# Performance work log

Measured on AMD Instinct MI355X. Metric: run time of the kernel, lower is better.

The kernel has to match this reference:

```python
import jax, jax.numpy as jnp
import numpy as np

EMBED = 1024
HEADS = 16
HEAD_DIM = EMBED // HEADS


def setup_inputs() -> dict:
    key = jax.random.key(0)
    ks = jax.random.split(key, 7)
    N, S = 2, 2048
    k = jax.random.normal(ks[0], (N, S, EMBED), dtype=jnp.float32)
    q = jax.random.normal(ks[1], (N, S, EMBED), dtype=jnp.float32)
    v = jax.random.normal(ks[2], (N, S, EMBED), dtype=jnp.float32)
    sc = 1.0 / np.sqrt(HEAD_DIM)
    # nn.Linear weights, applied as x @ W.T
    Wk = jax.random.normal(ks[3], (HEAD_DIM, HEAD_DIM), dtype=jnp.float32) * sc
    Wq = jax.random.normal(ks[4], (HEAD_DIM, HEAD_DIM), dtype=jnp.float32) * sc
    Wv = jax.random.normal(ks[5], (HEAD_DIM, HEAD_DIM), dtype=jnp.float32) * sc
    Wo = jax.random.normal(ks[6], (EMBED, EMBED), dtype=jnp.float32) / np.sqrt(EMBED)
    return {"k": k, "q": q, "v": v, "Wk": Wk, "Wq": Wq, "Wv": Wv, "Wo": Wo}


def reference(k, q, v, Wk, Wq, Wv, Wo):
    N, S, _ = q.shape
    # reshape to [N, S, H, D]; per-head projection weights shared across heads
    kh = jnp.einsum('nshd,ed->nshe', k.reshape(N, S, HEADS, HEAD_DIM), Wk)
    qh = jnp.einsum('nshd,ed->nshe', q.reshape(N, S, HEADS, HEAD_DIM), Wq)
    vh = jnp.einsum('nshd,ed->nshe', v.reshape(N, S, HEADS, HEAD_DIM), Wv)
    # energy: [N, H, q_len, k_len]
    energy = jnp.einsum('nqhd,nkhd->nhqk', qh, kh)
    attn = jax.nn.softmax(energy / jnp.sqrt(jnp.float32(HEAD_DIM)), axis=-1)
    out = jnp.einsum('nhqk,nkhd->nqhd', attn, vh).reshape(N, S, EMBED)
    return out @ Wo.T
```

## Files before the change

### kernel.cpp

```cpp
#include <hip/hip_runtime.h>

#define SQ   2048
#define HEADS 16
#define HD   64
#define EMB  1024

typedef __attribute__((ext_vector_type(2))) __fp16 h2;
typedef __attribute__((ext_vector_type(4))) __fp16 h4;
typedef __attribute__((ext_vector_type(8))) __fp16 h8;
typedef __attribute__((ext_vector_type(4))) float f4;
typedef unsigned short USH;
typedef unsigned int   UI;

__device__ __forceinline__ UI pkh(float a, float b) {
    h2 v = __builtin_amdgcn_cvt_pkrtz(a, b);
    return __builtin_bit_cast(UI, v);
}

__device__ __forceinline__ void glds16(const void* g, void* l) {
    __builtin_amdgcn_global_load_lds(
        (const __attribute__((address_space(1))) unsigned int*)g,
        (__attribute__((address_space(3))) unsigned int*)l, 16, 0, 0);
}

__global__ __launch_bounds__(256) void proj_fused(
    const float* __restrict__ q_in, const float* __restrict__ k_in,
    const float* __restrict__ v_in, const float* __restrict__ Wq,
    const float* __restrict__ Wk,   const float* __restrict__ Wv,
    const float* __restrict__ Wo,
    USH* __restrict__ Qh, USH* __restrict__ Kh, USH* __restrict__ Vt,
    USH* __restrict__ Wob)
{
    int t = threadIdx.x;
    if (blockIdx.y == 3) {
        int i = blockIdx.x * 256 + t;
        for (int j = 0; j < 4; ++j) {
            float4 v = ((const float4*)Wo)[i + j * 65536];
            uint2 pk; pk.x = pkh(v.x, v.y); pk.y = pkh(v.z, v.w);
            *(uint2*)(Wob + ((size_t)i + (size_t)j * 65536) * 4) = pk;
        }
        return;
    }
    const float* X = (blockIdx.y == 0) ? q_in : (blockIdx.y == 1) ? k_in : v_in;
    const float* W = (blockIdx.y == 0) ? Wq   : (blockIdx.y == 1) ? Wk   : Wv;
    float scale    = (blockIdx.y == 0) ? 0.18033688011112043f : 1.0f;

    __shared__ __align__(16) USH Xl[256][72];
    __shared__ __align__(16) USH Wl[64][72];

    const float4* Xg = (const float4*)(X + (size_t)blockIdx.x * 16384);
    for (int j = 0; j < 16; ++j) {
        int f = t + j * 256;
        float4 v = Xg[f];
        int row = f >> 4; int col = (f & 15) << 2;
        uint2 pk; pk.x = pkh(v.x, v.y); pk.y = pkh(v.z, v.w);
        *(uint2*)&Xl[row][col] = pk;
    }
    const float4* Wg = (const float4*)W;
    for (int j = 0; j < 4; ++j) {
        int f = t + j * 256;
        float4 v = Wg[f];
        int row = f >> 4; int col = (f & 15) << 2;
        uint2 pk; pk.x = pkh(v.x, v.y); pk.y = pkh(v.z, v.w);
        *(uint2*)&Wl[row][col] = pk;
    }
    __syncthreads();

    int wv = t >> 6, lane = t & 63, l4 = lane & 15, quad = lane >> 4;

    h8 wf[4][2], xf[4][2];
    for (int et = 0; et < 4; ++et)
        for (int ks = 0; ks < 2; ++ks)
            wf[et][ks] = *(const h8*)&Wl[et * 16 + l4][ks * 32 + quad * 8];
    for (int rt = 0; rt < 4; ++rt)
        for (int ks = 0; ks < 2; ++ks)
            xf[rt][ks] = *(const h8*)&Xl[wv * 64 + rt * 16 + l4][ks * 32 + quad * 8];

    f4 acc[4][4];
    for (int et = 0; et < 4; ++et)
        for (int rt = 0; rt < 4; ++rt) acc[et][rt] = (f4)(0.0f);
    for (int et = 0; et < 4; ++et)
        for (int rt = 0; rt < 4; ++rt)
            for (int ks = 0; ks < 2; ++ks)
                acc[et][rt] = __builtin_amdgcn_mfma_f32_16x16x32_f16(
                    wf[et][ks], xf[rt][ks], acc[et][rt], 0, 0, 0);

    if (blockIdx.y == 2) {
        int ns0 = blockIdx.x * 16 + wv * 4;
        int n = ns0 >> 11, s = ns0 & 2047;
        for (int et = 0; et < 4; ++et)
            for (int j = 0; j < 4; ++j) {
                int e = et * 16 + quad * 4 + j;
                uint2 pk;
                pk.x = pkh(acc[et][0][j], acc[et][1][j]);
                pk.y = pkh(acc[et][2][j], acc[et][3][j]);
                *(uint2*)(Vt + (((size_t)(n * HEADS + l4) * HD + e) * SQ + s)) = pk;
            }
    } else {
        USH* Out = (blockIdx.y == 0) ? Qh : Kh;
        for (int rt = 0; rt < 4; ++rt) {
            int ns = blockIdx.x * 16 + wv * 4 + rt;
            int n = ns >> 11, s = ns & 2047;
            USH* ob = Out + (((size_t)(n * HEADS) + l4) * SQ + s) * HD;
            for (int et = 0; et < 4; ++et) {
                uint2 pk;
                pk.x = pkh(acc[et][rt][0] * scale, acc[et][rt][1] * scale);
                pk.y = pkh(acc[et][rt][2] * scale, acc[et][rt][3] * scale);
                *(uint2*)(ob + et * 16 + quad * 4) = pk;
            }
        }
    }
}

__device__ __forceinline__ void stage_kv(const USH* __restrict__ Kg,
                                         const USH* __restrict__ Vg,
                                         int kt, USH* Kd, USH* Vd,
                                         int w, int lane)
{
#pragma unroll
    for (int j = 0; j < 2; ++j) {
        int s = (w * 2 + j) * 64 + lane;
        int r = s >> 3, c = (s & 7) ^ (r & 7);
        glds16(Kg + kt * 4096 + r * 64 + c * 8, Kd + s * 8);
    }
#pragma unroll
    for (int j = 0; j < 2; ++j) {
        int s = (w * 2 + j) * 64 + lane;
        int r = s >> 3, c = (s & 7) ^ (r & 7);
        glds16(Vg + r * SQ + kt * 64 + c * 8, Vd + s * 8);
    }
}

__global__ __launch_bounds__(256, 3) void attn_kernel(
    const USH* __restrict__ Qh, const USH* __restrict__ Kh,
    const USH* __restrict__ Vt, USH* __restrict__ Oh)
{
    __shared__ union {
        struct { USH K[2][4096]; USH V[2][4096]; } s;
        struct { float Osum[64][68]; float Lsum[64]; } r;
    } lds;

    int t = threadIdx.x, w = t >> 6, lane = t & 63;
    int l4 = lane & 15, quad = lane >> 4;
    int b = blockIdx.x;
    int nh = b & 31;
    int q0 = (b >> 5) * 64;
    const USH* Qg = Qh + ((size_t)nh * SQ + q0) * HD;
    const USH* Kg = Kh + (size_t)nh * SQ * HD;
    const USH* Vg = Vt + (size_t)nh * HD * SQ;

    h8 bq[4][2];
#pragma unroll
    for (int qt = 0; qt < 4; ++qt)
#pragma unroll
        for (int ks = 0; ks < 2; ++ks)
            bq[qt][ks] = *(const h8*)(Qg + (size_t)(qt * 16 + l4) * HD + ks * 32 + quad * 8);

    f4 o[4][4];
#pragma unroll
    for (int dt = 0; dt < 4; ++dt)
#pragma unroll
        for (int qt = 0; qt < 4; ++qt) o[dt][qt] = (f4)(0.0f);
    float lsum[4] = {0.f, 0.f, 0.f, 0.f};

    int key = w * 16 + l4;
    int kslot0 = key * 8 + (quad ^ (key & 7));
    int kslot1 = key * 8 + ((4 + quad) ^ (key & 7));
    int dchunk = w * 2 + (quad >> 1);
    int vbyte  = (quad & 1) * 4;

    stage_kv(Kg, Vg, 0, lds.s.K[0], lds.s.V[0], w, lane);

    for (int kt = 0; kt < SQ / 64; ++kt) {
        int cur = kt & 1;
        __syncthreads();
        if (kt + 1 < SQ / 64)
            stage_kv(Kg, Vg, kt + 1, lds.s.K[cur ^ 1], lds.s.V[cur ^ 1], w, lane);

        h8 ak0 = *(const h8*)(lds.s.K[cur] + kslot0 * 8);
        h8 ak1 = *(const h8*)(lds.s.K[cur] + kslot1 * 8);

        f4 sc[4];
#pragma unroll
        for (int qt = 0; qt < 4; ++qt) {
            f4 s0 = __builtin_amdgcn_mfma_f32_16x16x32_f16(ak0, bq[qt][0], (f4)(0.0f), 0, 0, 0);
            sc[qt] = __builtin_amdgcn_mfma_f32_16x16x32_f16(ak1, bq[qt][1], s0, 0, 0, 0);
        }

        h4 av[4];
#pragma unroll
        for (int dt = 0; dt < 4; ++dt) {
            int d = dt * 16 + l4;
            int vs = d * 8 + (dchunk ^ (d & 7));
            av[dt] = *(const h4*)(lds.s.V[cur] + vs * 8 + vbyte);
        }

        h4 p[4];
#pragma unroll
        for (int qt = 0; qt < 4; ++qt) {
            float p0 = __builtin_amdgcn_exp2f(sc[qt][0]);
            float p1 = __builtin_amdgcn_exp2f(sc[qt][1]);
            float p2 = __builtin_amdgcn_exp2f(sc[qt][2]);
            float p3 = __builtin_amdgcn_exp2f(sc[qt][3]);
            lsum[qt] += (p0 + p1) + (p2 + p3);
            uint2 u; u.x = pkh(p0, p1); u.y = pkh(p2, p3);
            p[qt] = __builtin_bit_cast(h4, u);
        }

#pragma unroll
        for (int dt = 0; dt < 4; ++dt)
#pragma unroll
            for (int qt = 0; qt < 4; ++qt)
                o[dt][qt] = __builtin_amdgcn_mfma_f32_16x16x16f16(
                    av[dt], p[qt], o[dt][qt], 0, 0, 0);
    }

#pragma unroll
    for (int qt = 0; qt < 4; ++qt) {
        lsum[qt] += __shfl_xor(lsum[qt], 16, 64);
        lsum[qt] += __shfl_xor(lsum[qt], 32, 64);
    }

    __syncthreads();
    for (int ph = 0; ph < 4; ++ph) {
        if (w == ph) {
            for (int dt = 0; dt < 4; ++dt)
                for (int qt = 0; qt < 4; ++qt) {
                    float* dst = &lds.r.Osum[qt * 16 + l4][dt * 16 + quad * 4];
                    f4 val = o[dt][qt];
                    if (ph) val += *(const f4*)dst;
                    *(f4*)dst = val;
                }
            if (quad == 0)
                for (int qt = 0; qt < 4; ++qt) {
                    int qi = qt * 16 + l4;
                    lds.r.Lsum[qi] = ph ? (lds.r.Lsum[qi] + lsum[qt]) : lsum[qt];
                }
        }
        __syncthreads();
    }

    int n = nh >> 4, h = nh & 15;
    int q = t >> 2, d0 = (t & 3) * 16;
    float inv = 1.0f / lds.r.Lsum[q];
    float vv[16];
#pragma unroll
    for (int i = 0; i < 4; ++i) {
        f4 x = *(const f4*)&lds.r.Osum[q][d0 + i * 4];
        vv[i * 4 + 0] = x[0] * inv; vv[i * 4 + 1] = x[1] * inv;
        vv[i * 4 + 2] = x[2] * inv; vv[i * 4 + 3] = x[3] * inv;
    }
    uint4 ou0, ou1;
    ou0.x = pkh(vv[0], vv[1]);   ou0.y = pkh(vv[2], vv[3]);
    ou0.z = pkh(vv[4], vv[5]);   ou0.w = pkh(vv[6], vv[7]);
    ou1.x = pkh(vv[8], vv[9]);   ou1.y = pkh(vv[10], vv[11]);
    ou1.z = pkh(vv[12], vv[13]); ou1.w = pkh(vv[14], vv[15]);
    USH* ob = Oh + ((size_t)(n * SQ + q0 + q)) * EMB + h * HD + d0;
    *(uint4*)ob = ou0;
    *(uint4*)(ob + 8) = ou1;
}

__global__ __launch_bounds__(256, 4) void gemm_bt(const USH* __restrict__ A,
                                                  const USH* __restrict__ B,
                                                  float* __restrict__ C)
{
    __shared__ __align__(16) USH Al[2][4096];
    __shared__ __align__(16) USH Bl[2][4096];
    int t = threadIdx.x, w = t >> 6, lane = t & 63;
    int l4 = lane & 15, quad = lane >> 4;
    int b = blockIdx.x;
    int m0 = (b & 63) * 64;
    int n0 = (b >> 6) * 64;
    int wm = (w >> 1) * 32, wn = (w & 1) * 32;

    f4 acc[2][2];
    for (int mt = 0; mt < 2; ++mt)
        for (int nt = 0; nt < 2; ++nt) acc[mt][nt] = (f4)(0.0f);

    int aslot[2][2], bslot[2][2];
#pragma unroll
    for (int mt = 0; mt < 2; ++mt)
#pragma unroll
        for (int ks = 0; ks < 2; ++ks) {
            int m = wm + mt * 16 + l4;
            aslot[mt][ks] = m * 8 + ((ks * 4 + quad) ^ (m & 7));
            int nn = wn + mt * 16 + l4;
            bslot[mt][ks] = nn * 8 + ((ks * 4 + quad) ^ (nn & 7));
        }

#pragma unroll
    for (int j = 0; j < 2; ++j) {
        int s = (w * 2 + j) * 64 + lane;
        int r = s >> 3, c = (s & 7) ^ (r & 7);
        glds16(A + (size_t)(m0 + r) * 1024 + c * 8, Al[0] + s * 8);
        glds16(B + (size_t)(n0 + r) * 1024 + c * 8, Bl[0] + s * 8);
    }

    for (int ki = 0; ki < 16; ++ki) {
        int cur = ki & 1;
        __syncthreads();
        if (ki + 1 < 16) {
            int k0 = (ki + 1) * 64;
#pragma unroll
            for (int j = 0; j < 2; ++j) {
                int s = (w * 2 + j) * 64 + lane;
                int r = s >> 3, c = (s & 7) ^ (r & 7);
                glds16(A + (size_t)(m0 + r) * 1024 + k0 + c * 8, Al[cur ^ 1] + s * 8);
                glds16(B + (size_t)(n0 + r) * 1024 + k0 + c * 8, Bl[cur ^ 1] + s * 8);
            }
        }

        h8 a[2][2], bf[2][2];
#pragma unroll
        for (int mt = 0; mt < 2; ++mt)
#pragma unroll
            for (int ks = 0; ks < 2; ++ks) {
                a[mt][ks]  = *(const h8*)(Al[cur] + aslot[mt][ks] * 8);
                bf[mt][ks] = *(const h8*)(Bl[cur] + bslot[mt][ks] * 8);
            }
#pragma unroll
        for (int mt = 0; mt < 2; ++mt)
#pragma unroll
            for (int nt = 0; nt < 2; ++nt)
#pragma unroll
                for (int ks = 0; ks < 2; ++ks)
                    acc[mt][nt] = __builtin_amdgcn_mfma_f32_16x16x32_f16(
                        a[mt][ks], bf[nt][ks], acc[mt][nt], 0, 0, 0);
    }

    for (int mt = 0; mt < 2; ++mt)
        for (int nt = 0; nt < 2; ++nt)
            for (int r = 0; r < 4; ++r)
                C[(size_t)(m0 + wm + mt * 16 + quad * 4 + r) * 1024 +
                  (n0 + wn + nt * 16 + l4)] = acc[mt][nt][r];
}

extern "C" void kernel_launch(void* const* d_in, const int* in_sizes, int n_in,
                              void* d_out, int out_size, void* d_ws, size_t ws_size,
                              hipStream_t stream) {
    const float* k_in = (const float*)d_in[0];
    const float* q_in = (const float*)d_in[1];
    const float* v_in = (const float*)d_in[2];
    const float* Wk   = (const float*)d_in[3];
    const float* Wq   = (const float*)d_in[4];
    const float* Wv   = (const float*)d_in[5];
    const float* Wo   = (const float*)d_in[6];
    float* out = (float*)d_out;

    char* ws = (char*)d_ws;
    USH* Qh  = (USH*)(ws);
    USH* Kh  = (USH*)(ws + 8388608);
    USH* Vt  = (USH*)(ws + 16777216);
    USH* Oh  = (USH*)(ws + 25165824);
    USH* Wob = (USH*)(ws + 33554432);

    proj_fused<<<dim3(256, 4), dim3(256), 0, stream>>>(
        q_in, k_in, v_in, Wq, Wk, Wv, Wo, Qh, Kh, Vt, Wob);
    attn_kernel<<<dim3(1024), dim3(256), 0, stream>>>(Qh, Kh, Vt, Oh);
    gemm_bt<<<dim3(1024), dim3(256), 0, stream>>>(Oh, Wob, out);
}
```

Before: 187.7 us.

## Load K/V fragments directly from global into registers, drop LDS staging and barriers

The attention kernel no longer stages K and V tiles in shared memory through async global-to-LDS loads with a barrier each iteration. Each wave now loads its own K and V MFMA fragments straight from global memory into registers, with a two-stage register double buffer (A/B) so the next tile's loads are issued before the current tile's compute. This removes per-iteration __syncthreads and LDS traffic, at the cost of uncoalesced, narrower global loads that rely on L2 hits and on more registers. The projection kernel also remaps blockIdx.x to interleave row blocks, which changes block scheduling order and write locality.

```diff
diff --git a/kernel.cpp b/kernel.cpp
--- a/kernel.cpp
+++ b/kernel.cpp
@@ -45,10 +45,12 @@
     const float* W = (blockIdx.y == 0) ? Wq   : (blockIdx.y == 1) ? Wk   : Wv;
     float scale    = (blockIdx.y == 0) ? 0.18033688011112043f : 1.0f;
 
+    int bx = (blockIdx.x & 7) * 32 + (blockIdx.x >> 3);
+
     __shared__ __align__(16) USH Xl[256][72];
     __shared__ __align__(16) USH Wl[64][72];
 
-    const float4* Xg = (const float4*)(X + (size_t)blockIdx.x * 16384);
+    const float4* Xg = (const float4*)(X + (size_t)bx * 16384);
     for (int j = 0; j < 16; ++j) {
         int f = t + j * 256;
         float4 v = Xg[f];
@@ -86,7 +88,7 @@
                     wf[et][ks], xf[rt][ks], acc[et][rt], 0, 0, 0);
 
     if (blockIdx.y == 2) {
-        int ns0 = blockIdx.x * 16 + wv * 4;
+        int ns0 = bx * 16 + wv * 4;
         int n = ns0 >> 11, s = ns0 & 2047;
         for (int et = 0; et < 4; ++et)
             for (int j = 0; j < 4; ++j) {
@@ -99,7 +101,7 @@
     } else {
         USH* Out = (blockIdx.y == 0) ? Qh : Kh;
         for (int rt = 0; rt < 4; ++rt) {
-            int ns = blockIdx.x * 16 + wv * 4 + rt;
+            int ns = bx * 16 + wv * 4 + rt;
             int n = ns >> 11, s = ns & 2047;
             USH* ob = Out + (((size_t)(n * HEADS) + l4) * SQ + s) * HD;
             for (int et = 0; et < 4; ++et) {
@@ -112,33 +114,11 @@
     }
 }
 
-__device__ __forceinline__ void stage_kv(const USH* __restrict__ Kg,
-                                         const USH* __restrict__ Vg,
-                                         int kt, USH* Kd, USH* Vd,
-                                         int w, int lane)
-{
-#pragma unroll
-    for (int j = 0; j < 2; ++j) {
-        int s = (w * 2 + j) * 64 + lane;
-        int r = s >> 3, c = (s & 7) ^ (r & 7);
-        glds16(Kg + kt * 4096 + r * 64 + c * 8, Kd + s * 8);
-    }
-#pragma unroll
-    for (int j = 0; j < 2; ++j) {
-        int s = (w * 2 + j) * 64 + lane;
-        int r = s >> 3, c = (s & 7) ^ (r & 7);
-        glds16(Vg + r * SQ + kt * 64 + c * 8, Vd + s * 8);
-    }
-}
-
 __global__ __launch_bounds__(256, 3) void attn_kernel(
     const USH* __restrict__ Qh, const USH* __restrict__ Kh,
     const USH* __restrict__ Vt, USH* __restrict__ Oh)
 {
-    __shared__ union {
-        struct { USH K[2][4096]; USH V[2][4096]; } s;
-        struct { float Osum[64][68]; float Lsum[64]; } r;
-    } lds;
+    __shared__ struct { float Osum[64][68]; float Lsum[64]; } lds;
 
     int t = threadIdx.x, w = t >> 6, lane = t & 63;
     int l4 = lane & 15, quad = lane >> 4;
@@ -163,57 +143,58 @@
         for (int qt = 0; qt < 4; ++qt) o[dt][qt] = (f4)(0.0f);
     float lsum[4] = {0.f, 0.f, 0.f, 0.f};
 
-    int key = w * 16 + l4;
-    int kslot0 = key * 8 + (quad ^ (key & 7));
-    int kslot1 = key * 8 + ((4 + quad) ^ (key & 7));
-    int dchunk = w * 2 + (quad >> 1);
-    int vbyte  = (quad & 1) * 4;
-
-    stage_kv(Kg, Vg, 0, lds.s.K[0], lds.s.V[0], w, lane);
-
-    for (int kt = 0; kt < SQ / 64; ++kt) {
-        int cur = kt & 1;
-        __syncthreads();
-        if (kt + 1 < SQ / 64)
-            stage_kv(Kg, Vg, kt + 1, lds.s.K[cur ^ 1], lds.s.V[cur ^ 1], w, lane);
-
-        h8 ak0 = *(const h8*)(lds.s.K[cur] + kslot0 * 8);
-        h8 ak1 = *(const h8*)(lds.s.K[cur] + kslot1 * 8);
-
-        f4 sc[4];
-#pragma unroll
-        for (int qt = 0; qt < 4; ++qt) {
-            f4 s0 = __builtin_amdgcn_mfma_f32_16x16x32_f16(ak0, bq[qt][0], (f4)(0.0f), 0, 0, 0);
-            sc[qt] = __builtin_amdgcn_mfma_f32_16x16x32_f16(ak1, bq[qt][1], s0, 0, 0, 0);
-        }
-
-        h4 av[4];
-#pragma unroll
-        for (int dt = 0; dt < 4; ++dt) {
-            int d = dt * 16 + l4;
-            int vs = d * 8 + (dchunk ^ (d & 7));
-            av[dt] = *(const h4*)(lds.s.V[cur] + vs * 8 + vbyte);
-        }
-
-        h4 p[4];
-#pragma unroll
-        for (int qt = 0; qt < 4; ++qt) {
-            float p0 = __builtin_amdgcn_exp2f(sc[qt][0]);
-            float p1 = __builtin_amdgcn_exp2f(sc[qt][1]);
-            float p2 = __builtin_amdgcn_exp2f(sc[qt][2]);
-            float p3 = __builtin_amdgcn_exp2f(sc[qt][3]);
-            lsum[qt] += (p0 + p1) + (p2 + p3);
-            uint2 u; u.x = pkh(p0, p1); u.y = pkh(p2, p3);
-            p[qt] = __builtin_bit_cast(h4, u);
-        }
-
-#pragma unroll
-        for (int dt = 0; dt < 4; ++dt)
-#pragma unroll
-            for (int qt = 0; qt < 4; ++qt)
-                o[dt][qt] = __builtin_amdgcn_mfma_f32_16x16x16f16(
-                    av[dt], p[qt], o[dt][qt], 0, 0, 0);
-    }
+    const USH* kp = Kg + (size_t)(w * 16 + l4) * HD + quad * 8;
+    const USH* vp = Vg + (size_t)l4 * SQ + w * 16 + quad * 4;
+
+#define ATTN_STEP(ak, av)                                                      \
+    {                                                                          \
+        h4 p[4];                                                               \
+        _Pragma("unroll")                                                      \
+        for (int qt = 0; qt < 4; ++qt) {                                       \
+            f4 s0 = __builtin_amdgcn_mfma_f32_16x16x32_f16(ak[0], bq[qt][0],   \
+                                                           (f4)(0.0f),0,0,0);  \
+            f4 sc = __builtin_amdgcn_mfma_f32_16x16x32_f16(ak[1], bq[qt][1],   \
+                                                           s0, 0, 0, 0);       \
+            float p0 = __builtin_amdgcn_exp2f(sc[0]);                          \
+            float p1 = __builtin_amdgcn_exp2f(sc[1]);                          \
+            float p2 = __builtin_amdgcn_exp2f(sc[2]);                          \
+            float p3 = __builtin_amdgcn_exp2f(sc[3]);                          \
+            lsum[qt] += (p0 + p1) + (p2 + p3);                                 \
+            uint2 u; u.x = pkh(p0, p1); u.y = pkh(p2, p3);                     \
+            p[qt] = __builtin_bit_cast(h4, u);                                 \
+        }                                                                      \
+        _Pragma("unroll")                                                      \
+        for (int dt = 0; dt < 4; ++dt)                                         \
+            _Pragma("unroll")                                                  \
+            for (int qt = 0; qt < 4; ++qt)                                     \
+                o[dt][qt] = __builtin_amdgcn_mfma_f32_16x16x16f16(             \
+                    av[dt], p[qt], o[dt][qt], 0, 0, 0);                        \
+    }
+
+    h8 akA[2], akB[2];
+    h4 avA[4], avB[4];
+
+    akA[0] = *(const h8*)kp;  akA[1] = *(const h8*)(kp + 32);
+    avA[0] = *(const h4*)vp;            avA[1] = *(const h4*)(vp + 16 * SQ);
+    avA[2] = *(const h4*)(vp + 32 * SQ); avA[3] = *(const h4*)(vp + 48 * SQ);
+
+    for (int kt = 0; kt < 32; kt += 2) {
+        const USH* kpB = kp + 4096;
+        const USH* vpB = vp + 64;
+        akB[0] = *(const h8*)kpB;  akB[1] = *(const h8*)(kpB + 32);
+        avB[0] = *(const h4*)vpB;             avB[1] = *(const h4*)(vpB + 16 * SQ);
+        avB[2] = *(const h4*)(vpB + 32 * SQ); avB[3] = *(const h4*)(vpB + 48 * SQ);
+
+        ATTN_STEP(akA, avA)
+
+        kp += 8192; vp += 128;
+        akA[0] = *(const h8*)kp;  akA[1] = *(const h8*)(kp + 32);
+        avA[0] = *(const h4*)vp;             avA[1] = *(const h4*)(vp + 16 * SQ);
+        avA[2] = *(const h4*)(vp + 32 * SQ); avA[3] = *(const h4*)(vp + 48 * SQ);
+
+        ATTN_STEP(akB, avB)
+    }
+#undef ATTN_STEP
 
 #pragma unroll
     for (int qt = 0; qt < 4; ++qt) {
@@ -226,7 +207,7 @@
         if (w == ph) {
             for (int dt = 0; dt < 4; ++dt)
                 for (int qt = 0; qt < 4; ++qt) {
-                    float* dst = &lds.r.Osum[qt * 16 + l4][dt * 16 + quad * 4];
+                    float* dst = &lds.Osum[qt * 16 + l4][dt * 16 + quad * 4];
                     f4 val = o[dt][qt];
                     if (ph) val += *(const f4*)dst;
                     *(f4*)dst = val;
@@ -234,7 +215,7 @@
             if (quad == 0)
                 for (int qt = 0; qt < 4; ++qt) {
                     int qi = qt * 16 + l4;
-                    lds.r.Lsum[qi] = ph ? (lds.r.Lsum[qi] + lsum[qt]) : lsum[qt];
+                    lds.Lsum[qi] = ph ? (lds.Lsum[qi] + lsum[qt]) : lsum[qt];
                 }
         }
         __syncthreads();
@@ -242,11 +223,11 @@
 
     int n = nh >> 4, h = nh & 15;
     int q = t >> 2, d0 = (t & 3) * 16;
-    float inv = 1.0f / lds.r.Lsum[q];
+    float inv = 1.0f / lds.Lsum[q];
     float vv[16];
 #pragma unroll
     for (int i = 0; i < 4; ++i) {
-        f4 x = *(const f4*)&lds.r.Osum[q][d0 + i * 4];
+        f4 x = *(const f4*)&lds.Osum[q][d0 + i * 4];
         vv[i * 4 + 0] = x[0] * inv; vv[i * 4 + 1] = x[1] * inv;
         vv[i * 4 + 2] = x[2] * inv; vv[i * 4 + 3] = x[3] * inv;
     }
```

After: 241.0 us. 28.4% more time.
